# Performance work log

Hardware: AMD Instinct MI355X
Metric: run time of the kernel (lower is better)

## Reference

```python
import jax, jax.numpy as jnp
import numpy as np

HEADS = 16

def setup_inputs() -> dict:
    key = jax.random.key(0)
    k1, k2, k3 = jax.random.split(key, 3)
    B, S, D = 2, 2048, 1024
    return {
        "query": jax.random.normal(k1, (B, S, D), dtype=jnp.float32),
        "key": jax.random.normal(k2, (B, S, D), dtype=jnp.float32),
        "value": jax.random.normal(k3, (B, S, D), dtype=jnp.float32),
    }

def reference(query, key, value):
    B, S, D = query.shape
    H = HEADS
    dh = D // H
    # split(-1) into H equal chunks == reshape to (B, S, H, dh)
    q = query.reshape(B, S, H, dh)
    k = key.reshape(B, S, H, dh)
    v = value.reshape(B, S, H, dh)
    scale = 1.0 / jnp.sqrt(jnp.asarray(dh, dtype=query.dtype))
    scores = jnp.einsum('bqhd,bkhd->bhqk', q, k) * scale  # [B,H,S,S]
    probs = jax.nn.softmax(scores, axis=-1)
    out = jnp.einsum('bhqk,bkhd->bqhd', probs, v)  # [B,S,H,dh]
    return out.reshape(B, S, D)
```

## Files before the change

kernel.cpp:

```cpp
#include <hip/hip_runtime.h>
#include <stdint.h>


#define B_ 2
#define S_ 2048
#define D_ 1024
#define H_ 16
#define DH 64
#define M_TILE 128

#define N_TILE2 64
#define NITER2 (S_ / N_TILE2)
#define KT2 8192
#define BUF2 16384
#define LSH_OFF2 (4 * BUF2)
#define SMEM_MAIN (LSH_OFF2 + 512)
#define O_STRIDE 36

typedef __bf16 bf16;
typedef __bf16 bf16x8 __attribute__((ext_vector_type(8)));
typedef float floatx4 __attribute__((ext_vector_type(4)));

__device__ __forceinline__ float fast_exp2(float x) {
#if __has_builtin(__builtin_amdgcn_exp2f)
  return __builtin_amdgcn_exp2f(x);
#else
  return exp2f(x);
#endif
}

__global__ __launch_bounds__(512, 4)
void attn_fwd(const float* __restrict__ Qg, const float* __restrict__ Kg,
              const float* __restrict__ Vg, float* __restrict__ Og) {
  __shared__ __align__(16) unsigned char smem[SMEM_MAIN];
  float* Osh = (float*)smem;
  float* Lsh = (float*)(smem + LSH_OFF2);

  const int tid  = threadIdx.x;
  const int lane = tid & 63;
  const int wave = tid >> 6;
  const int kw   = wave & 1;
  const int qw   = wave >> 1;
  const int col  = lane & 15;
  const int quad = lane >> 4;

  const int bid      = blockIdx.x;
  const int head_lin = bid & 31;
  const int qtile    = bid >> 5;
  const int b        = head_lin >> 4;
  const int h        = head_lin & 15;

  const float QSCALE = 0.125f * 1.44269504088896340736f;

  bf16x8 Qf[2][2];
#pragma unroll
  for (int qt = 0; qt < 2; ++qt) {
    const float* base = Qg + (size_t)(b * S_ + qtile * M_TILE + qw * 32 + qt * 16 + col) * D_
                        + h * DH + quad * 8;
#pragma unroll
    for (int ks = 0; ks < 2; ++ks) {
      float4 x0 = *(const float4*)(base + ks * 32);
      float4 x1 = *(const float4*)(base + ks * 32 + 4);
      bf16x8 f;
      f[0] = (bf16)(x0.x * QSCALE); f[1] = (bf16)(x0.y * QSCALE);
      f[2] = (bf16)(x0.z * QSCALE); f[3] = (bf16)(x0.w * QSCALE);
      f[4] = (bf16)(x1.x * QSCALE); f[5] = (bf16)(x1.y * QSCALE);
      f[6] = (bf16)(x1.z * QSCALE); f[7] = (bf16)(x1.w * QSCALE);
      Qf[qt][ks] = f;
    }
  }

  floatx4 accO[4][2];
  float l_lane[2] = {0.f, 0.f};
#pragma unroll
  for (int ft = 0; ft < 4; ++ft)
#pragma unroll
    for (int qt = 0; qt < 2; ++qt) accO[ft][qt] = (floatx4)0.f;

  const int sub = lane >> 3;
  const int lo3 = lane & 7;
  const int krow = (wave << 3) + sub;
  const float* Ksrc = Kg + (size_t)(b * S_ + krow) * D_ + h * DH + lo3 * 8;
  const int g4 = ((wave >> 2) << 5) + ((wave & 3) << 2);
  const float* Vsrc = Vg + (size_t)(b * S_) * D_ + h * DH + lane;

  const int kwr_off = krow * 128 + ((lo3 ^ sub) << 4);
  const int vwr_off = KT2 + lane * 128 + ((wave ^ (lane & 7)) << 4);

  const int cq = col & 7;
  const int ka0_off = (kw * 32 + col) * 128 + ((quad ^ cq) << 4);
  const int ka1_off = (kw * 32 + col) * 128 + (((quad | 4) ^ cq) << 4);
  const int va0_off = KT2 + col * 128 + (((kw * 4 + quad) ^ cq) << 4);

  {
    float4 k0 = *(const float4*)(Ksrc);
    float4 k1 = *(const float4*)(Ksrc + 4);
    float vv[8];
#pragma unroll
    for (int p = 0; p < 8; ++p)
      vv[p] = Vsrc[(size_t)(g4 + (p & 3) + ((p >> 2) << 4)) * D_];
    bf16x8 kb = {(bf16)k0.x, (bf16)k0.y, (bf16)k0.z, (bf16)k0.w,
                 (bf16)k1.x, (bf16)k1.y, (bf16)k1.z, (bf16)k1.w};
    *(bf16x8*)(smem + kwr_off) = kb;
    bf16x8 vb = {(bf16)vv[0], (bf16)vv[1], (bf16)vv[2], (bf16)vv[3],
                 (bf16)vv[4], (bf16)vv[5], (bf16)vv[6], (bf16)vv[7]};
    *(bf16x8*)(smem + vwr_off) = vb;
  }
  __syncthreads();

  bf16x8 Pf[2];

  for (int it = 0; it < NITER2; ++it) {
    const int bc = (it & 3) * BUF2;
    const int bp = ((it - 1) & 3) * BUF2;
    const int bn = ((it + 1) & 3) * BUF2;

    float4 k0, k1; float vv[8];
    if (it + 1 < NITER2) {
      const size_t koff = (size_t)(it + 1) * N_TILE2 * D_;
      k0 = *(const float4*)(Ksrc + koff);
      k1 = *(const float4*)(Ksrc + koff + 4);
#pragma unroll
      for (int p = 0; p < 8; ++p)
        vv[p] = Vsrc[koff + (size_t)(g4 + (p & 3) + ((p >> 2) << 4)) * D_];
    }
    __builtin_amdgcn_sched_barrier(0);

    floatx4 accS[2][2];
    __builtin_amdgcn_s_setprio(1);
#pragma unroll
    for (int kt = 0; kt < 2; ++kt) {
      bf16x8 Ka0 = *(const bf16x8*)(smem + bc + ka0_off + kt * 2048);
      bf16x8 Ka1 = *(const bf16x8*)(smem + bc + ka1_off + kt * 2048);
#pragma unroll
      for (int qt = 0; qt < 2; ++qt) {
        floatx4 a = (floatx4)0.f;
        a = __builtin_amdgcn_mfma_f32_16x16x32_bf16(Ka0, Qf[qt][0], a, 0, 0, 0);
        a = __builtin_amdgcn_mfma_f32_16x16x32_bf16(Ka1, Qf[qt][1], a, 0, 0, 0);
        accS[kt][qt] = a;
      }
    }

    if (it > 0) {
#pragma unroll
      for (int ft = 0; ft < 4; ++ft) {
        bf16x8 Va = *(const bf16x8*)(smem + bp + va0_off + ft * 2048);
#pragma unroll
        for (int qt = 0; qt < 2; ++qt)
          accO[ft][qt] = __builtin_amdgcn_mfma_f32_16x16x32_bf16(Va, Pf[qt], accO[ft][qt], 0, 0, 0);
      }
    }
    __builtin_amdgcn_s_setprio(0);

#pragma unroll
    for (int qt = 0; qt < 2; ++qt) {
      float rs = 0.f;
#pragma unroll
      for (int kt = 0; kt < 2; ++kt)
#pragma unroll
        for (int r = 0; r < 4; ++r) {
          float p = fast_exp2(accS[kt][qt][r]);
          accS[kt][qt][r] = p;
          rs += p;
        }
      l_lane[qt] += rs;
    }
#pragma unroll
    for (int qt = 0; qt < 2; ++qt) {
      floatx4 p0 = accS[0][qt], p1 = accS[1][qt];
      bf16x8 f = {(bf16)p0[0], (bf16)p0[1], (bf16)p0[2], (bf16)p0[3],
                  (bf16)p1[0], (bf16)p1[1], (bf16)p1[2], (bf16)p1[3]};
      Pf[qt] = f;
    }
    __builtin_amdgcn_sched_barrier(0);

    if (it + 1 < NITER2) {
      bf16x8 kb = {(bf16)k0.x, (bf16)k0.y, (bf16)k0.z, (bf16)k0.w,
                   (bf16)k1.x, (bf16)k1.y, (bf16)k1.z, (bf16)k1.w};
      *(bf16x8*)(smem + bn + kwr_off) = kb;
      bf16x8 vb = {(bf16)vv[0], (bf16)vv[1], (bf16)vv[2], (bf16)vv[3],
                   (bf16)vv[4], (bf16)vv[5], (bf16)vv[6], (bf16)vv[7]};
      *(bf16x8*)(smem + bn + vwr_off) = vb;
    }
    __syncthreads();
  }

  {
    const int bp = ((NITER2 - 1) & 3) * BUF2;
    __builtin_amdgcn_s_setprio(1);
#pragma unroll
    for (int ft = 0; ft < 4; ++ft) {
      bf16x8 Va = *(const bf16x8*)(smem + bp + va0_off + ft * 2048);
#pragma unroll
      for (int qt = 0; qt < 2; ++qt)
        accO[ft][qt] = __builtin_amdgcn_mfma_f32_16x16x32_bf16(Va, Pf[qt], accO[ft][qt], 0, 0, 0);
    }
    __builtin_amdgcn_s_setprio(0);
  }
  __syncthreads();

  float l_red[2];
#pragma unroll
  for (int qt = 0; qt < 2; ++qt) {
    float s = l_lane[qt];
    s += __shfl_xor(s, 16);
    s += __shfl_xor(s, 32);
    l_red[qt] = s;
  }

  if (kw == 1) {
    float* r = Osh + (qw * 64 + lane) * O_STRIDE;
#pragma unroll
    for (int qt = 0; qt < 2; ++qt)
#pragma unroll
      for (int ft = 0; ft < 4; ++ft)
        *(floatx4*)(r + (qt * 4 + ft) * 4) = accO[ft][qt];
    if (quad == 0) {
#pragma unroll
      for (int qt = 0; qt < 2; ++qt)
        Lsh[qw * 32 + qt * 16 + col] = l_red[qt];
    }
  }
  __syncthreads();

  if (kw == 0) {
    const float* r = Osh + (qw * 64 + lane) * O_STRIDE;
    float rl[2];
#pragma unroll
    for (int qt = 0; qt < 2; ++qt)
      rl[qt] = 1.0f / (l_red[qt] + Lsh[qw * 32 + qt * 16 + col]);
#pragma unroll
    for (int qt = 0; qt < 2; ++qt) {
      const int q = qtile * M_TILE + qw * 32 + qt * 16 + col;
      float* dst = Og + (size_t)(b * S_ + q) * D_ + h * DH + quad * 4;
#pragma unroll
      for (int ft = 0; ft < 4; ++ft) {
        floatx4 o = (accO[ft][qt] + *(const floatx4*)(r + (qt * 4 + ft) * 4)) * rl[qt];
        *(floatx4*)(dst + ft * 16) = o;
      }
    }
  }
}

extern "C" void kernel_launch(void* const* d_in, const int* in_sizes, int n_in,
                              void* d_out, int out_size, void* d_ws, size_t ws_size,
                              hipStream_t stream) {
  const float* Q = (const float*)d_in[0];
  const float* K = (const float*)d_in[1];
  const float* V = (const float*)d_in[2];
  float* O = (float*)d_out;
  (void)d_ws; (void)ws_size;
  hipLaunchKernelGGL(attn_fwd, dim3(B_ * H_ * (S_ / M_TILE)), dim3(512), 0, stream,
                     Q, K, V, O);
}
```

Measured before the change: 126.7 us.

## Deepen K/V prefetch to two tiles ahead with ping-pong register sets

Measured after the change: 140.3 us. +10.7%, slower.

```diff
diff --git a/kernel.cpp b/kernel.cpp
--- a/kernel.cpp
+++ b/kernel.cpp
@@ -92,39 +92,28 @@
   const int ka1_off = (kw * 32 + col) * 128 + (((quad | 4) ^ cq) << 4);
   const int va0_off = KT2 + col * 128 + (((kw * 4 + quad) ^ cq) << 4);
 
-  {
-    float4 k0 = *(const float4*)(Ksrc);
-    float4 k1 = *(const float4*)(Ksrc + 4);
-    float vv[8];
+  auto issue_loads = [&](int tile, float4& k0, float4& k1, float* vv) {
+    const size_t koff = (size_t)tile * N_TILE2 * D_;
+    k0 = *(const float4*)(Ksrc + koff);
+    k1 = *(const float4*)(Ksrc + koff + 4);
 #pragma unroll
     for (int p = 0; p < 8; ++p)
-      vv[p] = Vsrc[(size_t)(g4 + (p & 3) + ((p >> 2) << 4)) * D_];
+      vv[p] = Vsrc[koff + (size_t)(g4 + (p & 3) + ((p >> 2) << 4)) * D_];
+  };
+  auto write_stage = [&](int bufoff, const float4& k0, const float4& k1, const float* vv) {
     bf16x8 kb = {(bf16)k0.x, (bf16)k0.y, (bf16)k0.z, (bf16)k0.w,
                  (bf16)k1.x, (bf16)k1.y, (bf16)k1.z, (bf16)k1.w};
-    *(bf16x8*)(smem + kwr_off) = kb;
+    *(bf16x8*)(smem + bufoff + kwr_off) = kb;
     bf16x8 vb = {(bf16)vv[0], (bf16)vv[1], (bf16)vv[2], (bf16)vv[3],
                  (bf16)vv[4], (bf16)vv[5], (bf16)vv[6], (bf16)vv[7]};
-    *(bf16x8*)(smem + vwr_off) = vb;
-  }
-  __syncthreads();
+    *(bf16x8*)(smem + bufoff + vwr_off) = vb;
+  };
 
   bf16x8 Pf[2];
 
-  for (int it = 0; it < NITER2; ++it) {
+  auto compute_iter = [&](int it) {
     const int bc = (it & 3) * BUF2;
     const int bp = ((it - 1) & 3) * BUF2;
-    const int bn = ((it + 1) & 3) * BUF2;
-
-    float4 k0, k1; float vv[8];
-    if (it + 1 < NITER2) {
-      const size_t koff = (size_t)(it + 1) * N_TILE2 * D_;
-      k0 = *(const float4*)(Ksrc + koff);
-      k1 = *(const float4*)(Ksrc + koff + 4);
-#pragma unroll
-      for (int p = 0; p < 8; ++p)
-        vv[p] = Vsrc[koff + (size_t)(g4 + (p & 3) + ((p >> 2) << 4)) * D_];
-    }
-    __builtin_amdgcn_sched_barrier(0);
 
     floatx4 accS[2][2];
     __builtin_amdgcn_s_setprio(1);
@@ -140,7 +129,6 @@
         accS[kt][qt] = a;
       }
     }
-
     if (it > 0) {
 #pragma unroll
       for (int ft = 0; ft < 4; ++ft) {
@@ -151,7 +139,6 @@
       }
     }
     __builtin_amdgcn_s_setprio(0);
-
 #pragma unroll
     for (int qt = 0; qt < 2; ++qt) {
       float rs = 0.f;
@@ -172,17 +159,40 @@
                   (bf16)p1[0], (bf16)p1[1], (bf16)p1[2], (bf16)p1[3]};
       Pf[qt] = f;
     }
-    __builtin_amdgcn_sched_barrier(0);
-
-    if (it + 1 < NITER2) {
-      bf16x8 kb = {(bf16)k0.x, (bf16)k0.y, (bf16)k0.z, (bf16)k0.w,
-                   (bf16)k1.x, (bf16)k1.y, (bf16)k1.z, (bf16)k1.w};
-      *(bf16x8*)(smem + bn + kwr_off) = kb;
-      bf16x8 vb = {(bf16)vv[0], (bf16)vv[1], (bf16)vv[2], (bf16)vv[3],
-                   (bf16)vv[4], (bf16)vv[5], (bf16)vv[6], (bf16)vv[7]};
-      *(bf16x8*)(smem + bn + vwr_off) = vb;
-    }
-    __syncthreads();
+  };
+
+  float4 kA0, kA1, kB0, kB1;
+  float vvA[8], vvB[8];
+
+  {
+    float4 k0 = *(const float4*)(Ksrc);
+    float4 k1 = *(const float4*)(Ksrc + 4);
+    float vv[8];
+#pragma unroll
+    for (int p = 0; p < 8; ++p)
+      vv[p] = Vsrc[(size_t)(g4 + (p & 3) + ((p >> 2) << 4)) * D_];
+    write_stage(0, k0, k1, vv);
+  }
+  issue_loads(1, kA0, kA1, vvA);
+  __syncthreads();
+
+  for (int itp = 0; itp < NITER2; itp += 2) {
+    {
+      const int it = itp;
+      write_stage(((it + 1) & 3) * BUF2, kA0, kA1, vvA);
+      if (it + 2 < NITER2) issue_loads(it + 2, kB0, kB1, vvB);
+      __builtin_amdgcn_sched_barrier(0);
+      compute_iter(it);
+      __syncthreads();
+    }
+    {
+      const int it = itp + 1;
+      if (it + 1 < NITER2) write_stage(((it + 1) & 3) * BUF2, kB0, kB1, vvB);
+      if (it + 2 < NITER2) issue_loads(it + 2, kA0, kA1, vvA);
+      __builtin_amdgcn_sched_barrier(0);
+      compute_iter(it);
+      __syncthreads();
+    }
   }
 
   {
```
